# Performance work log

Measured on AMD Instinct MI355X. Metric: run time of the kernel, lower is better.

The kernel has to match this reference:

```python
import jax, jax.numpy as jnp
import numpy as np

EPS = float(np.finfo(np.float32).eps)

# (joint_id, joint_name, parent_name) in the module's fkm_computation_order
ORDER = [
    (1, 'rHip', 'hip'), (2, 'rKnee', 'rHip'), (3, 'rAnkle', 'rKnee'), (4, 'rToe', 'rAnkle'),
    (6, 'lHip', 'hip'), (7, 'lKnee', 'lHip'), (8, 'lAnkle', 'lKnee'), (9, 'lToe', 'lAnkle'),
    (11, 'spine', 'hip'), (12, 'spine1', 'spine'), (13, 'thorax', 'spine1'), (14, 'neck', 'thorax'),
    (15, 'head', 'neck'), (16, 'lShoulderAnchor', 'spine1'), (17, 'lShoulder', 'lShoulderAnchor'),
    (18, 'lElbow', 'lShoulder'), (19, 'lWrist', 'lElbow'), (20, 'lThumb', 'lWrist'),
    (22, 'lWristEnd', 'lWrist'), (24, 'rShoulderAnchor', 'spine1'), (25, 'rShoulder', 'rShoulderAnchor'),
    (26, 'rElbow', 'rShoulder'), (27, 'rWrist', 'rElbow'), (28, 'rThumb', 'rWrist'),
    (30, 'rWristEnd', 'rWrist'),
]


def axis_angle_to_matrix(a):
    """Rodrigues formula, batched. a: [B,3] -> [B,3,3]."""
    theta = jnp.linalg.norm(a, axis=-1, keepdims=True)  # [B,1]
    r = a / (theta + EPS)                               # [B,3]
    r0, r1, r2 = r[:, 0], r[:, 1], r[:, 2]
    z = jnp.zeros_like(r0)
    # skew-symmetric S with S[0,1]=-r2, S[0,2]=r1, S[1,2]=-r0 (as in torch code)
    S = jnp.stack([
        jnp.stack([z, -r2, r1], axis=-1),
        jnp.stack([r2, z, -r0], axis=-1),
        jnp.stack([-r1, r0, z], axis=-1),
    ], axis=-2)  # [B,3,3]
    th = theta[..., None]  # [B,1,1]
    I = jnp.eye(3, dtype=a.dtype)
    return I + jnp.sin(th) * S + (1.0 - jnp.cos(th)) * (S @ S)


def setup_inputs() -> dict:
    key = jax.random.key(0)
    k1, k2 = jax.random.split(key)
    B = 262144
    x = jax.random.normal(k1, (B, 99), dtype=jnp.float32)
    offset = jax.random.normal(k2, (32, 3), dtype=jnp.float32)
    return {"x": x, "offset": offset}


def reference(x, offset):
    # hip root: position from first 3 dims, orientation from dims 3:6
    pos = {"hip": offset[0] + x[:, 0:3]}                # [B,3]
    ang = {"hip": axis_angle_to_matrix(x[:, 3:6])}      # [B,3,3]
    # local rotations for every joint in the chain: dims [3*id+3 : 3*id+6]
    local = {name: axis_angle_to_matrix(x[:, 3 * i + 3: 3 * i + 6]) for i, name, _ in ORDER}
    # sequential forward kinematics down the tree
    for i, cur, par in ORDER:
        # offset[i] @ R_parent  (row-vector times matrix), then translate
        pos[cur] = jnp.einsum('j,bjk->bk', offset[i], ang[par]) + pos[par]
        ang[cur] = local[cur] @ ang[par]
    # positions in the same order as get_joint_positions(): hip then chain order
    return jnp.stack([pos['hip']] + [pos[c] for _, c, _ in ORDER], axis=1)  # [B,26,3]
```

## Files before the change

kernel.cpp:

```cpp
#include <hip/hip_runtime.h>

#define RPB  64
#define TPB  64
#define XDIM 99
#define NJ   26
#define OUTW 78
#define CH   32

__device__ __forceinline__ float fast_rcp(float a)  { return __builtin_amdgcn_rcpf(a); }
__device__ __forceinline__ float fast_sqrt(float a) { return __builtin_amdgcn_sqrtf(a); }

__device__ __forceinline__ void rodrigues(float ax, float ay, float az, float* R) {
    const float EPS = 1.1920928955078125e-07f;
    float t = fast_sqrt(ax*ax + ay*ay + az*az);
    float inv = fast_rcp(t + EPS);
    float r0 = ax*inv, r1 = ay*inv, r2 = az*inv;
    float s, c;
    __sincosf(t, &s, &c);
    float omc = 1.0f - c;
    float r00 = r0*r0, r11 = r1*r1, r22 = r2*r2;
    float r01 = r0*r1, r02 = r0*r2, r12 = r1*r2;
    R[0] = 1.0f - omc*(r11 + r22);
    R[1] = -s*r2 + omc*r01;
    R[2] =  s*r1 + omc*r02;
    R[3] =  s*r2 + omc*r01;
    R[4] = 1.0f - omc*(r00 + r22);
    R[5] = -s*r0 + omc*r12;
    R[6] = -s*r1 + omc*r02;
    R[7] =  s*r0 + omc*r12;
    R[8] = 1.0f - omc*(r00 + r11);
}

__global__ __launch_bounds__(TPB, 3) void skel_fk(const float* __restrict__ x,
                                                  const float* __restrict__ off,
                                                  float* __restrict__ out) {
    __shared__ float tb[CH * OUTW];
    const int l = threadIdx.x;
    const int row0 = blockIdx.x * RPB;
    const float* rp = x + (long long)(row0 + l) * XDIM;

    constexpr int OFF_IDX[NJ] = {0,1,2,3,4,6,7,8,9,11,12,13,14,15,16,17,18,19,20,22,24,25,26,27,28,30};
    constexpr int PAR[NJ]     = {-1,0,1,2,3,0,5,6,7,0,9,10,11,12,10,14,15,16,17,17,10,20,21,22,23,23};

    float ang[NJ][9];
    float pp[NJ][3];

    {
        float R[9];
        rodrigues(rp[3], rp[4], rp[5], R);
        #pragma unroll
        for (int q = 0; q < 9; ++q) ang[0][q] = R[q];
        pp[0][0] = off[0] + rp[0];
        pp[0][1] = off[1] + rp[1];
        pp[0][2] = off[2] + rp[2];
    }

    #pragma unroll
    for (int s = 1; s < NJ; ++s) {
        const int i  = OFF_IDX[s];
        const int pa = PAR[s];
        float L[9];
        rodrigues(rp[3*i+3], rp[3*i+4], rp[3*i+5], L);
        const float o0 = off[3*i], o1 = off[3*i+1], o2 = off[3*i+2];
        #pragma unroll
        for (int c = 0; c < 3; ++c)
            pp[s][c] = o0*ang[pa][c] + o1*ang[pa][3+c] + o2*ang[pa][6+c] + pp[pa][c];
        #pragma unroll
        for (int j = 0; j < 3; ++j)
            #pragma unroll
            for (int kk = 0; kk < 3; ++kk)
                ang[s][3*j+kk] = L[3*j+0]*ang[pa][0+kk]
                               + L[3*j+1]*ang[pa][3+kk]
                               + L[3*j+2]*ang[pa][6+kk];
    }

    #pragma unroll
    for (int c = 0; c < 2; ++c) {
        if (c) __syncthreads();
        if ((l >> 5) == c) {
            float* srow = &tb[(l & 31) * OUTW];
            #pragma unroll
            for (int j = 0; j < 39; ++j) {
                float2 v;
                v.x = pp[(2*j)   / 3][(2*j)   % 3];
                v.y = pp[(2*j+1) / 3][(2*j+1) % 3];
                *reinterpret_cast<float2*>(&srow[2*j]) = v;
            }
        }
        __syncthreads();
        float* ob = out + ((long long)row0 + CH * c) * OUTW;
        #pragma unroll
        for (int j = 0; j < 20; ++j) {
            int m = l + j * TPB;
            if (m < CH * OUTW / 2) {
                float2 v = *reinterpret_cast<const float2*>(&tb[2*m]);
                *reinterpret_cast<float2*>(&ob[2*m]) = v;
            }
        }
    }
}

extern "C" void kernel_launch(void* const* d_in, const int* in_sizes, int n_in,
                              void* d_out, int out_size, void* d_ws, size_t ws_size,
                              hipStream_t stream) {
    const float* x   = (const float*)d_in[0];
    const float* off = (const float*)d_in[1];
    float* out = (float*)d_out;
    const int B = in_sizes[0] / XDIM;
    const int grid = B / RPB;
    skel_fk<<<grid, TPB, 0, stream>>>(x, off, out);
}
```

Measured before the change: 40.81 us.

## Stage input rows through LDS with coalesced direct-to-LDS loads in two halves

Replaces the per-thread strided row reads of x (99-float stride) with coalesced global_load_lds transfers into shared memory. This is done in two halves of 49 columns so the LDS footprint stays small, and joints are split into two compute phases to match. The output staging uses a padded stride of 79 with scalar stores, and the block barriers are replaced by waitcnt plus sched_barrier, which is only safe because the block is a single wavefront. The goal is better global memory coalescing. The cost is extra LDS traffic and the serialisation introduced by the two load phases.

```diff
diff --git a/kernel.cpp b/kernel.cpp
--- a/kernel.cpp
+++ b/kernel.cpp
@@ -1,11 +1,12 @@
 #include <hip/hip_runtime.h>
 
-#define RPB  64
-#define TPB  64
-#define XDIM 99
-#define NJ   26
-#define OUTW 78
-#define CH   32
+#define TPB   64
+#define RPW   64
+#define XDIM  99
+#define NJ    26
+#define OUTW  78
+#define LSTR  49
+#define SSTR  79
 
 __device__ __forceinline__ float fast_rcp(float a)  { return __builtin_amdgcn_rcpf(a); }
 __device__ __forceinline__ float fast_sqrt(float a) { return __builtin_amdgcn_sqrtf(a); }
@@ -34,33 +35,47 @@
 __global__ __launch_bounds__(TPB, 3) void skel_fk(const float* __restrict__ x,
                                                   const float* __restrict__ off,
                                                   float* __restrict__ out) {
-    __shared__ float tb[CH * OUTW];
+    __shared__ float buf[RPW * LSTR];
     const int l = threadIdx.x;
-    const int row0 = blockIdx.x * RPB;
-    const float* rp = x + (long long)(row0 + l) * XDIM;
+    const int row0 = blockIdx.x * RPW;
+    const float* xb = x + (long long)row0 * XDIM;
 
     constexpr int OFF_IDX[NJ] = {0,1,2,3,4,6,7,8,9,11,12,13,14,15,16,17,18,19,20,22,24,25,26,27,28,30};
     constexpr int PAR[NJ]     = {-1,0,1,2,3,0,5,6,7,0,9,10,11,12,10,14,15,16,17,17,10,20,21,22,23,23};
 
+    #pragma unroll
+    for (int j = 0; j < 49; ++j) {
+        const int f = l + 64 * j;
+        const int r = f / LSTR;
+        const int c = f - LSTR * r;
+        __builtin_amdgcn_global_load_lds(
+            (const __attribute__((address_space(1))) unsigned int*)(xb + 99*r + c),
+            (__attribute__((address_space(3))) unsigned int*)(buf + 64*j),
+            4, 0, 0);
+    }
+    asm volatile("s_waitcnt vmcnt(0)" ::: "memory");
+    __builtin_amdgcn_sched_barrier(0);
+
+    const float* row = &buf[l * LSTR];
     float ang[NJ][9];
     float pp[NJ][3];
 
     {
         float R[9];
-        rodrigues(rp[3], rp[4], rp[5], R);
+        rodrigues(row[3], row[4], row[5], R);
         #pragma unroll
         for (int q = 0; q < 9; ++q) ang[0][q] = R[q];
-        pp[0][0] = off[0] + rp[0];
-        pp[0][1] = off[1] + rp[1];
-        pp[0][2] = off[2] + rp[2];
+        pp[0][0] = off[0] + row[0];
+        pp[0][1] = off[1] + row[1];
+        pp[0][2] = off[2] + row[2];
     }
-
     #pragma unroll
-    for (int s = 1; s < NJ; ++s) {
+    for (int s = 1; s <= 12; ++s) {
         const int i  = OFF_IDX[s];
         const int pa = PAR[s];
+        const int col = 3*i + 3;
         float L[9];
-        rodrigues(rp[3*i+3], rp[3*i+4], rp[3*i+5], L);
+        rodrigues(row[col], row[col+1], row[col+2], L);
         const float o0 = off[3*i], o1 = off[3*i+1], o2 = off[3*i+2];
         #pragma unroll
         for (int c = 0; c < 3; ++c)
@@ -73,29 +88,63 @@
                                + L[3*j+1]*ang[pa][3+kk]
                                + L[3*j+2]*ang[pa][6+kk];
     }
+    __builtin_amdgcn_sched_barrier(0);
 
     #pragma unroll
-    for (int c = 0; c < 2; ++c) {
-        if (c) __syncthreads();
-        if ((l >> 5) == c) {
-            float* srow = &tb[(l & 31) * OUTW];
+    for (int j = 0; j < 49; ++j) {
+        const int f = l + 64 * j;
+        const int r = f / LSTR;
+        const int c = f - LSTR * r;
+        __builtin_amdgcn_global_load_lds(
+            (const __attribute__((address_space(1))) unsigned int*)(xb + 99*r + 48 + c),
+            (__attribute__((address_space(3))) unsigned int*)(buf + 64*j),
+            4, 0, 0);
+    }
+    asm volatile("s_waitcnt vmcnt(0)" ::: "memory");
+    __builtin_amdgcn_sched_barrier(0);
+
+    #pragma unroll
+    for (int s = 13; s < NJ; ++s) {
+        const int i  = OFF_IDX[s];
+        const int pa = PAR[s];
+        const int col = 3*i + 3 - 48;
+        float L[9];
+        rodrigues(row[col], row[col+1], row[col+2], L);
+        const float o0 = off[3*i], o1 = off[3*i+1], o2 = off[3*i+2];
+        #pragma unroll
+        for (int c = 0; c < 3; ++c)
+            pp[s][c] = o0*ang[pa][c] + o1*ang[pa][3+c] + o2*ang[pa][6+c] + pp[pa][c];
+        #pragma unroll
+        for (int j = 0; j < 3; ++j)
             #pragma unroll
-            for (int j = 0; j < 39; ++j) {
-                float2 v;
-                v.x = pp[(2*j)   / 3][(2*j)   % 3];
-                v.y = pp[(2*j+1) / 3][(2*j+1) % 3];
-                *reinterpret_cast<float2*>(&srow[2*j]) = v;
+            for (int kk = 0; kk < 3; ++kk)
+                ang[s][3*j+kk] = L[3*j+0]*ang[pa][0+kk]
+                               + L[3*j+1]*ang[pa][3+kk]
+                               + L[3*j+2]*ang[pa][6+kk];
+    }
+    __builtin_amdgcn_sched_barrier(0);
+
+    float* ob = out + (long long)row0 * OUTW;
+    #pragma unroll
+    for (int g2 = 0; g2 < 2; ++g2) {
+        __builtin_amdgcn_sched_barrier(0);
+        if ((l >> 5) == g2) {
+            float* srow = &buf[(l & 31) * SSTR];
+            #pragma unroll
+            for (int s = 0; s < NJ; ++s) {
+                srow[3*s+0] = pp[s][0];
+                srow[3*s+1] = pp[s][1];
+                srow[3*s+2] = pp[s][2];
             }
         }
-        __syncthreads();
-        float* ob = out + ((long long)row0 + CH * c) * OUTW;
+        asm volatile("s_waitcnt lgkmcnt(0)" ::: "memory");
+        __builtin_amdgcn_sched_barrier(0);
         #pragma unroll
-        for (int j = 0; j < 20; ++j) {
-            int m = l + j * TPB;
-            if (m < CH * OUTW / 2) {
-                float2 v = *reinterpret_cast<const float2*>(&tb[2*m]);
-                *reinterpret_cast<float2*>(&ob[2*m]) = v;
-            }
+        for (int j = 0; j < 39; ++j) {
+            const int m = l + 64 * j;
+            const int r = m / OUTW;
+            const int c = m - OUTW * r;
+            ob[g2 * (32 * OUTW) + m] = buf[r * SSTR + c];
         }
     }
 }
@@ -107,6 +156,6 @@
     const float* off = (const float*)d_in[1];
     float* out = (float*)d_out;
     const int B = in_sizes[0] / XDIM;
-    const int grid = B / RPB;
+    const int grid = B / RPW;
     skel_fk<<<grid, TPB, 0, stream>>>(x, off, out);
 }
```

Measured after the change: 113.1 us. 177% more time.

## Stage input rows into LDS via global_load_lds and widen output stores

Applied to the files above, without the earlier changes.

Each block now copies its 64 input rows into shared memory with coalesced direct global-to-LDS loads, instead of having each thread read its own strided row from global memory. The shared buffer is then reused to stage all 64 output rows at once, written back with float4 stores in place of two half-block float2 passes. This targets uncoalesced global reads and the extra synchronisation of the old output path. In exchange it uses more LDS per block (about 25KB) while raising the launch-bounds occupancy hint, and LDS reads with a 99-float row stride may cause bank conflicts.

```diff
diff --git a/kernel.cpp b/kernel.cpp
--- a/kernel.cpp
+++ b/kernel.cpp
@@ -1,11 +1,10 @@
 #include <hip/hip_runtime.h>
 
-#define RPB  64
-#define TPB  64
-#define XDIM 99
-#define NJ   26
-#define OUTW 78
-#define CH   32
+#define TPB   64
+#define RPW   64
+#define XDIM  99
+#define NJ    26
+#define OUTW  78
 
 __device__ __forceinline__ float fast_rcp(float a)  { return __builtin_amdgcn_rcpf(a); }
 __device__ __forceinline__ float fast_sqrt(float a) { return __builtin_amdgcn_sqrtf(a); }
@@ -31,13 +30,31 @@
     R[8] = 1.0f - omc*(r00 + r11);
 }
 
-__global__ __launch_bounds__(TPB, 3) void skel_fk(const float* __restrict__ x,
+__global__ __launch_bounds__(TPB, 4) void skel_fk(const float* __restrict__ x,
                                                   const float* __restrict__ off,
                                                   float* __restrict__ out) {
-    __shared__ float tb[CH * OUTW];
+    __shared__ __align__(16) float buf[RPW * XDIM];
     const int l = threadIdx.x;
-    const int row0 = blockIdx.x * RPB;
-    const float* rp = x + (long long)(row0 + l) * XDIM;
+    const int row0 = blockIdx.x * RPW;
+    const float* gsrc = x + (long long)row0 * XDIM;
+
+    #pragma unroll
+    for (int j = 0; j < 24; ++j) {
+        __builtin_amdgcn_global_load_lds(
+            (const __attribute__((address_space(1))) unsigned int*)(gsrc + 256*j + 4*l),
+            (__attribute__((address_space(3))) unsigned int*)(buf + 256*j),
+            16, 0, 0);
+    }
+    #pragma unroll
+    for (int kk = 0; kk < 3; ++kk) {
+        __builtin_amdgcn_global_load_lds(
+            (const __attribute__((address_space(1))) unsigned int*)(gsrc + 6144 + 64*kk + l),
+            (__attribute__((address_space(3))) unsigned int*)(buf + 6144 + 64*kk),
+            4, 0, 0);
+    }
+    __syncthreads();
+
+    const float* row = &buf[l * XDIM];
 
     constexpr int OFF_IDX[NJ] = {0,1,2,3,4,6,7,8,9,11,12,13,14,15,16,17,18,19,20,22,24,25,26,27,28,30};
     constexpr int PAR[NJ]     = {-1,0,1,2,3,0,5,6,7,0,9,10,11,12,10,14,15,16,17,17,10,20,21,22,23,23};
@@ -47,12 +64,12 @@
 
     {
         float R[9];
-        rodrigues(rp[3], rp[4], rp[5], R);
+        rodrigues(row[3], row[4], row[5], R);
         #pragma unroll
         for (int q = 0; q < 9; ++q) ang[0][q] = R[q];
-        pp[0][0] = off[0] + rp[0];
-        pp[0][1] = off[1] + rp[1];
-        pp[0][2] = off[2] + rp[2];
+        pp[0][0] = off[0] + row[0];
+        pp[0][1] = off[1] + row[1];
+        pp[0][2] = off[2] + row[2];
     }
 
     #pragma unroll
@@ -60,7 +77,7 @@
         const int i  = OFF_IDX[s];
         const int pa = PAR[s];
         float L[9];
-        rodrigues(rp[3*i+3], rp[3*i+4], rp[3*i+5], L);
+        rodrigues(row[3*i+3], row[3*i+4], row[3*i+5], L);
         const float o0 = off[3*i], o1 = off[3*i+1], o2 = off[3*i+2];
         #pragma unroll
         for (int c = 0; c < 3; ++c)
@@ -73,30 +90,29 @@
                                + L[3*j+1]*ang[pa][3+kk]
                                + L[3*j+2]*ang[pa][6+kk];
     }
+    __syncthreads();
 
-    #pragma unroll
-    for (int c = 0; c < 2; ++c) {
-        if (c) __syncthreads();
-        if ((l >> 5) == c) {
-            float* srow = &tb[(l & 31) * OUTW];
-            #pragma unroll
-            for (int j = 0; j < 39; ++j) {
-                float2 v;
-                v.x = pp[(2*j)   / 3][(2*j)   % 3];
-                v.y = pp[(2*j+1) / 3][(2*j+1) % 3];
-                *reinterpret_cast<float2*>(&srow[2*j]) = v;
-            }
+    {
+        float2* wr2 = reinterpret_cast<float2*>(buf) + 39 * l;
+        #pragma unroll
+        for (int j = 0; j < 39; ++j) {
+            float2 v;
+            v.x = pp[(2*j)   / 3][(2*j)   % 3];
+            v.y = pp[(2*j+1) / 3][(2*j+1) % 3];
+            wr2[j] = v;
         }
-        __syncthreads();
-        float* ob = out + ((long long)row0 + CH * c) * OUTW;
+    }
+    __syncthreads();
+
+    {
+        float4* ob4 = reinterpret_cast<float4*>(out + (long long)row0 * OUTW);
+        const float4* b4 = reinterpret_cast<const float4*>(buf);
         #pragma unroll
-        for (int j = 0; j < 20; ++j) {
-            int m = l + j * TPB;
-            if (m < CH * OUTW / 2) {
-                float2 v = *reinterpret_cast<const float2*>(&tb[2*m]);
-                *reinterpret_cast<float2*>(&ob[2*m]) = v;
-            }
-        }
+        for (int j = 0; j < 19; ++j)
+            ob4[l + 64*j] = b4[l + 64*j];
+        float2* ob2 = reinterpret_cast<float2*>(out + (long long)row0 * OUTW);
+        const float2* b2 = reinterpret_cast<const float2*>(buf);
+        ob2[2432 + l] = b2[2432 + l];
     }
 }
 
@@ -107,6 +123,6 @@
     const float* off = (const float*)d_in[1];
     float* out = (float*)d_out;
     const int B = in_sizes[0] / XDIM;
-    const int grid = B / RPB;
+    const int grid = B / RPW;
     skel_fk<<<grid, TPB, 0, stream>>>(x, off, out);
 }
```

Measured after the change: 39.78 us. 1.03x faster.
